# Optimization experiments

Hardware: AMD Instinct MI355X
Metric: run time of the kernel (lower is better)

The kernel has to match this reference:

```python
import jax, jax.numpy as jnp
import numpy as np


def _antideriv_tanh(t):
    # int tanh dx = |x| + log1p(exp(-2|x|))  (numerically stable)
    a = jnp.abs(t)
    return a + jnp.log1p(jnp.exp(-2.0 * a))


def _deriv_tanh(t):
    th = jnp.tanh(t)
    return 1.0 - th * th


def setup_inputs() -> dict:
    key = jax.random.key(0)
    ks = jax.random.split(key, 9)
    d, m, nTh, r, nex = 63, 256, 3, 10, 4096
    x = jax.random.normal(ks[0], (nex, d + 1), dtype=jnp.float32)
    W0 = jax.random.normal(ks[1], (m, d + 1), dtype=jnp.float32) / jnp.sqrt(float(d + 1))
    b0 = jax.random.normal(ks[2], (m,), dtype=jnp.float32) * 0.1
    Wd = jax.random.normal(ks[3], (nTh - 1, m, m), dtype=jnp.float32) / jnp.sqrt(float(m))
    bd = jax.random.normal(ks[4], (nTh - 1, m), dtype=jnp.float32) * 0.1
    wv = jax.random.normal(ks[5], (m,), dtype=jnp.float32)
    A = jax.random.normal(ks[6], (r, d + 1), dtype=jnp.float32) / jnp.sqrt(float(d + 1))
    cw = jax.random.normal(ks[7], (d + 1,), dtype=jnp.float32) * 0.1
    cb = jax.random.normal(ks[8], (), dtype=jnp.float32) * 0.1
    return {"x": x, "W0": W0, "b0": b0, "Wd": Wd, "bd": bd, "wv": wv, "A": A, "cw": cw, "cb": cb}


def reference(x, W0, b0, Wd, bd, wv, A, cw, cb):
    """Phi.trHess: returns (grad of Phi wrt x, trace of Hessian of Phi), shapes [nex, d+1], [nex]."""
    nTh = Wd.shape[0] + 1
    h = 1.0 / (nTh - 1)
    m = W0.shape[0]
    nex = x.shape[0]
    d = x.shape[1] - 1

    symA = A.T @ A                                  # [d+1, d+1]

    # ---- forward propagation of ResNN, keeping hidden states u and preactivations ----
    opening = x @ W0.T + b0                         # [nex, m]
    u = [_antideriv_tanh(opening)]
    pre = []                                        # preactivations of layers 1..nTh-1
    feat = u[0]
    for i in range(1, nTh):
        p = feat @ Wd[i - 1].T + bd[i - 1]          # [nex, m]
        pre.append(p)
        feat = feat + h * _antideriv_tanh(p)
        u.append(feat)

    tanhopen = jnp.tanh(opening)                    # [nex, m]

    # ---- backward z chain (Eq. 11): gradient of w'N(x) wrt x ----
    z = [None] * nTh
    for i in range(nTh - 1, 0, -1):
        term = wv[:, None] if i == nTh - 1 else z[i + 1]      # [m,1] or [m,nex]
        z[i] = term + h * (Wd[i - 1].T @ (jnp.tanh(pre[i - 1]).T * term))
    z0 = W0.T @ (tanhopen.T * z[1])                 # [d+1, nex]
    grad = z0 + symA @ x.T + cw[:, None]            # [d+1, nex]

    # ---- trace of Hessian (Eq. 13) ----
    Kopen = W0[:, :d]                               # [m, d]  (spatial part of opening weight)
    temp = _deriv_tanh(opening.T) * z[1]            # [m, nex]
    # sum_{m,d} temp[m,n] * Kopen[m,d]^2
    trH = jnp.einsum('mn,m->n', temp, jnp.sum(Kopen * Kopen, axis=1))

    Jac = Kopen[:, :, None] * tanhopen.T[:, None, :]          # [m, d, nex]
    for i in range(1, nTh):
        KJ = (Wd[i - 1] @ Jac.reshape(m, d * nex)).reshape(m, d, nex)
        term = wv[:, None] if i == nTh - 1 else z[i + 1]
        p = pre[i - 1].T                             # [m, nex]
        t_i = jnp.einsum('mn,mdn->n', _deriv_tanh(p) * term, KJ * KJ)
        trH = trH + h * t_i
        Jac = Jac + h * jnp.tanh(p)[:, None, :] * KJ

    trH = trH + jnp.trace(symA[:d, :d])
    return grad.T, trH
```

## Files before the change

kernel.cpp:

```cpp
#include <hip/hip_runtime.h>
#include <hip/hip_bf16.h>

#define NEX 4096
#define M   256
#define NM  (NEX*M)

typedef __attribute__((ext_vector_type(8))) short short8;
typedef __attribute__((ext_vector_type(16))) float floatx16;
typedef __attribute__((ext_vector_type(4))) unsigned short ushort4v;

__device__ inline unsigned short f2bfu(float x) {
    __hip_bfloat16 h = __float2bfloat16(x);
    union { __hip_bfloat16 b; unsigned short u; } cv; cv.b = h;
    return cv.u;
}
__device__ inline float bfu2f(unsigned short u) {
    union { unsigned short u; __hip_bfloat16 b; } cv; cv.u = u;
    return __bfloat162float(cv.b);
}

__global__ void k_prep(const float* __restrict__ Wd, const float* __restrict__ W0,
                       const float* __restrict__ A,
                       unsigned short* __restrict__ FB,
                       unsigned short* __restrict__ FBT,
                       unsigned short* __restrict__ FW0,
                       unsigned short* __restrict__ FWT,
                       unsigned short* __restrict__ FSA,
                       float* __restrict__ FA,
                       float* __restrict__ ksq, float* __restrict__ trace) {
    int b = blockIdx.x, t = threadIdx.x;
    int lane = t & 63, l31 = lane & 31, lhi = lane >> 5;
    if (b < 64) {
        int combo = b*4 + (t >> 6);
        int l = combo >> 7, rest = combo & 127;
        int mtile = rest >> 4, kstep = rest & 15;
        const float* src = Wd + l*65536 + (mtile*32 + l31)*256 + kstep*16 + lhi*8;
        int off = l*65536 + (mtile*16 + kstep)*512 + lane*8;
        #pragma unroll
        for (int e = 0; e < 8; ++e) FB[off+e] = f2bfu(src[e]);
    } else if (b < 128) {
        int combo = (b-64)*4 + (t >> 6);
        int l = combo >> 7, rest = combo & 127;
        int kt = rest >> 4, ms = rest & 15;
        const float* src = Wd + l*65536 + (ms*16 + lhi*8)*256 + kt*32 + l31;
        int off = l*65536 + (kt*16 + ms)*512 + lane*8;
        #pragma unroll
        for (int e = 0; e < 8; ++e) FBT[off+e] = f2bfu(src[e*256]);
    } else if (b < 136) {
        int combo = (b-128)*4 + (t >> 6);
        int mt = combo >> 2, ks = combo & 3;
        const float* src = W0 + (mt*32 + l31)*64 + ks*16 + lhi*8;
        int off = combo*512 + lane*8;
        #pragma unroll
        for (int e = 0; e < 8; ++e) FW0[off+e] = f2bfu(src[e]);
    } else if (b < 144) {
        int combo = (b-136)*4 + (t >> 6);
        int ct = combo >> 4, ms = combo & 15;
        const float* src = W0 + (ms*16 + lhi*8)*64 + ct*32 + l31;
        int off = combo*512 + lane*8;
        #pragma unroll
        for (int e = 0; e < 8; ++e) FWT[off+e] = f2bfu(src[e*64]);
    } else if (b < 146) {
        int combo = (b-144)*4 + (t >> 6);
        int ct = combo >> 2, ks = combo & 3;
        int c = ct*32 + l31;
        int off = combo*512 + lane*8;
        #pragma unroll
        for (int e = 0; e < 8; ++e) {
            int j = ks*16 + lhi*8 + e;
            float s = 0.f;
            #pragma unroll
            for (int r = 0; r < 10; ++r) s += A[r*64+c] * A[r*64+j];
            FSA[off+e] = f2bfu(s);
        }
    } else if (b == 146) {
        float s = 0.f;
        for (int dd = 0; dd < 63; dd++) { float v = W0[t*64+dd]; s += v*v; }
        ksq[t] = s;
        float p = 0.f;
        for (int idx = t; idx < 630; idx += 256) {
            int r = idx / 63, i = idx % 63;
            float v = A[r*64+i]; p += v*v;
        }
        for (int off = 32; off; off >>= 1) p += __shfl_down(p, off, 64);
        __shared__ float red[4];
        if ((t & 63) == 0) red[t >> 6] = p;
        __syncthreads();
        if (t == 0) trace[0] = red[0]+red[1]+red[2]+red[3];
    } else {
        int q = (b-147)*256 + t;
        int tl = q & 63, frag = q >> 6;
        int d  = (frag >> 4)*32 + (tl & 31);
        int m0 = (frag & 15)*16 + (tl >> 5)*8;
        float* dst = FA + q*8;
        #pragma unroll
        for (int e = 0; e < 8; ++e)
            dst[e] = (d == 63) ? 0.f : W0[(m0 + e)*64 + d];
    }
}

__global__ __launch_bounds__(512, 2) void k_fb(
        const float* __restrict__ x, const float* __restrict__ b0,
        const float* __restrict__ bd, const float* __restrict__ wv,
        const float* __restrict__ cw,
        const unsigned short* __restrict__ FW0,
        const unsigned short* __restrict__ FB,
        const unsigned short* __restrict__ FBT,
        const unsigned short* __restrict__ FWT,
        const unsigned short* __restrict__ FSA,
        float* __restrict__ tanhopen, float* __restrict__ tp0g,
        float* __restrict__ tp1g, float* __restrict__ z2T, float* __restrict__ z1T,
        float* __restrict__ out) {
    __shared__ __align__(16) unsigned short Buh[8192], Bul[8192];
    __shared__ __align__(16) unsigned short Bxh[2048], Bxl[2048];
    __shared__ __align__(16) float bounce[8224];
    __shared__ float b0s[256], bd0s[256], bd1s[256], wvs[256], cws[64];
    int n0 = blockIdx.x * 32, t = threadIdx.x;
    int lane = t & 63, w = t >> 6, l31 = lane & 31, lhi = lane >> 5;

    if (t < 256) { b0s[t]=b0[t]; bd0s[t]=bd[t]; bd1s[t]=bd[256+t]; wvs[t]=wv[t]; }
    if (t < 64) cws[t] = cw[t];
    if (t < 256) {
        int tl = t & 63;
        int ex = tl & 31, k0 = (t >> 6)*16 + (tl >> 5)*8;
        const float* xp = x + (n0+ex)*64 + k0;
        short8 h8, l8;
        #pragma unroll
        for (int e = 0; e < 8; ++e) {
            float v = xp[e];
            unsigned short h = f2bfu(v);
            h8[e] = (short)h; l8[e] = (short)f2bfu(v - bfu2f(h));
        }
        *reinterpret_cast<short8*>(&Bxh[t*8]) = h8;
        *reinterpret_cast<short8*>(&Bxl[t*8]) = l8;
    }
    __syncthreads();

#define MROW(r) (w*32 + ((r)&3) + 8*((r)>>2) + 4*lhi)

#define MFMA2(AH, BH, BL) do { \
    acc = __builtin_amdgcn_mfma_f32_32x32x16_bf16(AH, BH, acc, 0, 0, 0); \
    acc = __builtin_amdgcn_mfma_f32_32x32x16_bf16(AH, BL, acc, 0, 0, 0); \
} while (0)

#define GEMM256(PH) do { \
    for (int ks = 0; ks < 16; ++ks) { \
        short8 Ah = *reinterpret_cast<const short8*>(PH + (w*16+ks)*512 + lane*8); \
        short8 Bh = *reinterpret_cast<const short8*>(&Buh[(ks*64+lane)*8]); \
        short8 Bl = *reinterpret_cast<const short8*>(&Bul[(ks*64+lane)*8]); \
        MFMA2(Ah, Bh, Bl); \
    } \
} while (0)

#define EPILOGUE(SVAL, DST, BVAL) do { \
    __syncthreads(); \
    _Pragma("unroll") \
    for (int r = 0; r < 16; ++r) bounce[l31*257 + MROW(r)] = SVAL[r]; \
    _Pragma("unroll") \
    for (int g = 0; g < 4; ++g) { \
        int ks_ = w*2 + (g>>1); \
        int lp_ = (g&1)*32 + l31; \
        int base_ = (ks_*64 + lp_)*8 + 4*lhi; \
        ushort4v h4, l4; \
        _Pragma("unroll") \
        for (int q = 0; q < 4; ++q) { \
            float v_ = BVAL[g*4+q]; \
            unsigned short h_ = f2bfu(v_); \
            h4[q] = h_; l4[q] = f2bfu(v_ - bfu2f(h_)); \
        } \
        *reinterpret_cast<ushort4v*>(&Buh[base_]) = h4; \
        *reinterpret_cast<ushort4v*>(&Bul[base_]) = l4; \
    } \
    __syncthreads(); \
    _Pragma("unroll") \
    for (int i = 0; i < 16; ++i) { \
        int f = t + i*512; int ex_ = f >> 8, m_ = f & 255; \
        DST[(n0+ex_)*256 + m_] = bounce[ex_*257 + m_]; \
    } \
} while (0)

    floatx16 acc;
    float sv[16], u0v[16], tp0v[16], z2v[16], cf[16];

    #pragma unroll
    for (int r = 0; r < 16; ++r) acc[r] = 0.f;
    #pragma unroll
    for (int ks = 0; ks < 4; ++ks) {
        short8 Ah = *reinterpret_cast<const short8*>(FW0 + (w*4+ks)*512 + lane*8);
        short8 Bh = *reinterpret_cast<const short8*>(&Bxh[(ks*64+lane)*8]);
        short8 Bl = *reinterpret_cast<const short8*>(&Bxl[(ks*64+lane)*8]);
        MFMA2(Ah, Bh, Bl);
    }
    #pragma unroll
    for (int r = 0; r < 16; ++r) {
        float p = acc[r] + b0s[MROW(r)];
        float a = fabsf(p);
        float e = __expf(-2.f*a);
        float th = (1.f - e) * __builtin_amdgcn_rcpf(1.f + e);
        sv[r] = __builtin_copysignf(th, p);
        u0v[r] = a + __logf(1.f + e);
    }
    EPILOGUE(sv, tanhopen, u0v);

    #pragma unroll
    for (int r = 0; r < 16; ++r) acc[r] = 0.f;
    GEMM256(FB);
    #pragma unroll
    for (int r = 0; r < 16; ++r) {
        float p = acc[r] + bd0s[MROW(r)];
        float a = fabsf(p);
        float e = __expf(-2.f*a);
        float th = (1.f - e) * __builtin_amdgcn_rcpf(1.f + e);
        tp0v[r] = __builtin_copysignf(th, p);
        u0v[r] += 0.5f*(a + __logf(1.f + e));
    }
    EPILOGUE(tp0v, tp0g, u0v);

    #pragma unroll
    for (int r = 0; r < 16; ++r) acc[r] = 0.f;
    GEMM256(FB + 65536);
    #pragma unroll
    for (int r = 0; r < 16; ++r) {
        float p = acc[r] + bd1s[MROW(r)];
        float a = fabsf(p);
        float e = __expf(-2.f*a);
        float th = (1.f - e) * __builtin_amdgcn_rcpf(1.f + e);
        cf[r] = __builtin_copysignf(th, p);
        z2v[r] = cf[r] * wvs[MROW(r)];
    }
    EPILOGUE(cf, tp1g, z2v);

    #pragma unroll
    for (int r = 0; r < 16; ++r) acc[r] = 0.f;
    GEMM256(FBT + 65536);
    #pragma unroll
    for (int r = 0; r < 16; ++r) {
        z2v[r] = wvs[MROW(r)] + 0.5f*acc[r];
        cf[r] = tp0v[r] * z2v[r];
    }
    EPILOGUE(z2v, z2T, cf);

    #pragma unroll
    for (int r = 0; r < 16; ++r) acc[r] = 0.f;
    GEMM256(FBT);
    #pragma unroll
    for (int r = 0; r < 16; ++r) {
        z2v[r] += 0.5f*acc[r];
        cf[r] = sv[r] * z2v[r];
    }
    EPILOGUE(z2v, z1T, cf);

    {
        int ct = w >> 2, seg = w & 3;
        #pragma unroll
        for (int r = 0; r < 16; ++r) acc[r] = 0.f;
        #pragma unroll
        for (int k2 = 0; k2 < 4; ++k2) {
            int ms = seg*4 + k2;
            short8 Ah = *reinterpret_cast<const short8*>(FWT + (ct*16+ms)*512 + lane*8);
            short8 Bh = *reinterpret_cast<const short8*>(&Buh[(ms*64+lane)*8]);
            short8 Bl = *reinterpret_cast<const short8*>(&Bul[(ms*64+lane)*8]);
            MFMA2(Ah, Bh, Bl);
        }
        if (seg == 0) {
            #pragma unroll
            for (int ks = 0; ks < 4; ++ks) {
                short8 Ah = *reinterpret_cast<const short8*>(FSA + (ct*4+ks)*512 + lane*8);
                short8 Bh = *reinterpret_cast<const short8*>(&Bxh[(ks*64+lane)*8]);
                short8 Bl = *reinterpret_cast<const short8*>(&Bxl[(ks*64+lane)*8]);
                MFMA2(Ah, Bh, Bl);
            }
        }
        __syncthreads();
        float* gpart = bounce;
        #pragma unroll
        for (int r = 0; r < 16; ++r) gpart[w*1024 + (2*r+lhi)*32 + l31] = acc[r];
        __syncthreads();
        int o0 = t*4, ex = o0 >> 6, c0 = o0 & 63;
        float4 gv;
        #pragma unroll
        for (int jj = 0; jj < 4; ++jj) {
            int c = c0 + jj;
            int ctx = c >> 5, cr = c & 31;
            int lh = (cr >> 2) & 1;
            int rr = (cr & 3) | ((cr >> 3) << 2);
            float s = cws[c];
            #pragma unroll
            for (int sg = 0; sg < 4; ++sg)
                s += gpart[(ctx*4+sg)*1024 + (2*rr+lh)*32 + ex];
            gv[jj] = s;
        }
        *reinterpret_cast<float4*>(&out[(n0+ex)*64 + c0]) = gv;
    }
#undef MROW
#undef MFMA2
#undef GEMM256
#undef EPILOGUE
}

__global__ __launch_bounds__(256, 3) void k_heavy_mfma(
        const float* __restrict__ tanhopen, const float* __restrict__ tp0,
        const float* __restrict__ tp1, const float* __restrict__ z2T,
        const float* __restrict__ z1T, const float* __restrict__ wv,
        const float* __restrict__ FA, const unsigned short* __restrict__ FB,
        const float* __restrict__ ksq, const float* __restrict__ trace,
        float* __restrict__ outTrH) {
    __shared__ __align__(16) unsigned short Bf[16384];
    __shared__ float ss[256], tp0s[256], w1s[256], w2s[256];
    __shared__ float red[4];
    int n = blockIdx.x, t = threadIdx.x;
    int lane = t & 63, w = t >> 6, l31 = lane & 31, lhi = lane >> 5;

    float sv = tanhopen[n*256 + t];
    float a0 = tp0[n*256 + t];
    float a1 = tp1[n*256 + t];
    ss[t] = sv;
    tp0s[t] = a0;
    w1s[t] = (1.f - a0*a0) * z2T[n*256 + t];
    w2s[t] = (1.f - a1*a1) * wv[t];
    float tot = (1.f - sv*sv) * z1T[n*256 + t] * ksq[t];
    __syncthreads();

    #pragma unroll
    for (int i = 0; i < 8; ++i) {
        int q = t + i*256;
        int frag = q >> 6, tl = q & 63;
        int k0 = (frag & 15)*16 + (tl >> 5)*8;
        const float* fp = FA + q*8;
        short8 v8;
        #pragma unroll
        for (int e = 0; e < 8; ++e)
            v8[e] = (short)f2bfu(fp[e] * ss[k0 + e]);
        *reinterpret_cast<short8*>(&Bf[q*8]) = v8;
    }
    __syncthreads();

    floatx16 acc[2][2];
    int mt0 = w*2, mt1 = w*2 + 1;
    float wtot = 0.f;

    #pragma unroll
    for (int jm = 0; jm < 2; ++jm)
        #pragma unroll
        for (int dh = 0; dh < 2; ++dh)
            #pragma unroll
            for (int r = 0; r < 16; ++r) acc[jm][dh][r] = 0.f;

    for (int ks = 0; ks < 16; ++ks) {
        short8 A0 = *reinterpret_cast<const short8*>(FB + (mt0*16 + ks)*512 + lane*8);
        short8 A1 = *reinterpret_cast<const short8*>(FB + (mt1*16 + ks)*512 + lane*8);
        short8 B0 = *reinterpret_cast<const short8*>(&Bf[((ks)*64 + lane)*8]);
        short8 B1 = *reinterpret_cast<const short8*>(&Bf[((16 + ks)*64 + lane)*8]);
        acc[0][0] = __builtin_amdgcn_mfma_f32_32x32x16_bf16(A0, B0, acc[0][0], 0, 0, 0);
        acc[0][1] = __builtin_amdgcn_mfma_f32_32x32x16_bf16(A0, B1, acc[0][1], 0, 0, 0);
        acc[1][0] = __builtin_amdgcn_mfma_f32_32x32x16_bf16(A1, B0, acc[1][0], 0, 0, 0);
        acc[1][1] = __builtin_amdgcn_mfma_f32_32x32x16_bf16(A1, B1, acc[1][1], 0, 0, 0);
    }
    __syncthreads();

    #pragma unroll
    for (int jm = 0; jm < 2; ++jm) {
        int mt = w*2 + jm;
        #pragma unroll
        for (int g = 0; g < 4; ++g) {
            float w1m[4], tm[4];
            #pragma unroll
            for (int q = 0; q < 4; ++q) {
                int m = mt*32 + 8*g + q + 4*lhi;
                w1m[q] = 0.5f * w1s[m];
                tm[q]  = 0.5f * tp0s[m];
            }
            #pragma unroll
            for (int dh = 0; dh < 2; ++dh) {
                int base = ((dh*16 + mt*2 + (g >> 1))*64
                            + ((g & 1)*32 + l31))*8 + 4*lhi;
                ushort4v old = *reinterpret_cast<ushort4v*>(&Bf[base]);
                ushort4v nw;
                #pragma unroll
                for (int q = 0; q < 4; ++q) {
                    float v = acc[jm][dh][4*g + q];
                    wtot += w1m[q] * v * v;
                    nw[q] = f2bfu(bfu2f(old[q]) + tm[q] * v);
                }
                *reinterpret_cast<ushort4v*>(&Bf[base]) = nw;
            }
        }
    }
    __syncthreads();

    #pragma unroll
    for (int jm = 0; jm < 2; ++jm)
        #pragma unroll
        for (int dh = 0; dh < 2; ++dh)
            #pragma unroll
            for (int r = 0; r < 16; ++r) acc[jm][dh][r] = 0.f;

    const unsigned short* FB1 = FB + 65536;
    for (int ks = 0; ks < 16; ++ks) {
        short8 A0 = *reinterpret_cast<const short8*>(FB1 + (mt0*16 + ks)*512 + lane*8);
        short8 A1 = *reinterpret_cast<const short8*>(FB1 + (mt1*16 + ks)*512 + lane*8);
        short8 B0 = *reinterpret_cast<const short8*>(&Bf[((ks)*64 + lane)*8]);
        short8 B1 = *reinterpret_cast<const short8*>(&Bf[((16 + ks)*64 + lane)*8]);
        acc[0][0] = __builtin_amdgcn_mfma_f32_32x32x16_bf16(A0, B0, acc[0][0], 0, 0, 0);
        acc[0][1] = __builtin_amdgcn_mfma_f32_32x32x16_bf16(A0, B1, acc[0][1], 0, 0, 0);
        acc[1][0] = __builtin_amdgcn_mfma_f32_32x32x16_bf16(A1, B0, acc[1][0], 0, 0, 0);
        acc[1][1] = __builtin_amdgcn_mfma_f32_32x32x16_bf16(A1, B1, acc[1][1], 0, 0, 0);
    }

    #pragma unroll
    for (int jm = 0; jm < 2; ++jm)
        #pragma unroll
        for (int g = 0; g < 4; ++g)
            #pragma unroll
            for (int q = 0; q < 4; ++q) {
                int m = (w*2 + jm)*32 + 8*g + q + 4*lhi;
                float w2m = 0.5f * w2s[m];
                float v0 = acc[jm][0][4*g + q], v1 = acc[jm][1][4*g + q];
                wtot += w2m * (v0*v0 + v1*v1);
            }

    tot += wtot;

    for (int off = 32; off; off >>= 1) tot += __shfl_down(tot, off, 64);
    if (lane == 0) red[w] = tot;
    __syncthreads();
    if (t == 0) outTrH[n] = red[0] + red[1] + red[2] + red[3] + trace[0];
}


extern "C" void kernel_launch(void* const* d_in, const int* in_sizes, int n_in,
                              void* d_out, int out_size, void* d_ws, size_t ws_size,
                              hipStream_t stream) {
    const float* x   = (const float*)d_in[0];
    const float* W0  = (const float*)d_in[1];
    const float* b0  = (const float*)d_in[2];
    const float* Wd  = (const float*)d_in[3];
    const float* bd  = (const float*)d_in[4];
    const float* wv  = (const float*)d_in[5];
    const float* A   = (const float*)d_in[6];
    const float* cw  = (const float*)d_in[7];
    float* out = (float*)d_out;
    float* ws  = (float*)d_ws;

    float* tanhopen = ws;
    float* tp0  = tanhopen + NM;
    float* tp1  = tp0 + NM;
    float* z2T  = tp1 + NM;
    float* z1T  = z2T + NM;
    float* FA   = z1T + NM;
    float* ksq  = FA + 16384;
    float* trace= ksq + 256;
    unsigned short* FB  = (unsigned short*)(trace + 4);
    unsigned short* FBT = FB + 131072;
    unsigned short* FW0 = FBT + 131072;
    unsigned short* FWT = FW0 + 16384;
    unsigned short* FSA = FWT + 16384;

    k_prep<<<155, 256, 0, stream>>>(Wd, W0, A, FB, FBT, FW0, FWT, FSA,
                                    FA, ksq, trace);
    k_fb<<<NEX/32, 512, 0, stream>>>(x, b0, bd, wv, cw,
                                     FW0, FB, FBT, FWT, FSA,
                                     tanhopen, tp0, tp1, z2T, z1T, out);
    k_heavy_mfma<<<NEX, 256, 0, stream>>>(tanhopen, tp0, tp1, z2T, z1T, wv,
                                          FA, FB, ksq, trace, out + NEX*64);
}
```

Measured before the change: 121.1 us.

## Split heavy trace kernel across 8 waves with software-pipelined MFMA loads

Doubles the block size of the per-sample trace kernel from 4 to 8 waves, each wave now owning one 32-row M tile instead of two, which halves accumulator registers per wave. The MFMA loops are unrolled with double-buffered A/B fragment loads, and the first A fragments of the second GEMM are prefetched before the barrier. The aim is more waves in flight and better latency hiding of global and LDS loads. The cost is more threads per block sharing the same LDS and barriers, and half the threads sit idle during the initial staging.

```diff
diff --git a/kernel.cpp b/kernel.cpp
--- a/kernel.cpp
+++ b/kernel.cpp
@@ -298,7 +298,7 @@
 #undef EPILOGUE
 }
 
-__global__ __launch_bounds__(256, 3) void k_heavy_mfma(
+__global__ __launch_bounds__(512, 4) void k_heavy_mfma(
         const float* __restrict__ tanhopen, const float* __restrict__ tp0,
         const float* __restrict__ tp1, const float* __restrict__ z2T,
         const float* __restrict__ z1T, const float* __restrict__ wv,
@@ -307,25 +307,28 @@
         float* __restrict__ outTrH) {
     __shared__ __align__(16) unsigned short Bf[16384];
     __shared__ float ss[256], tp0s[256], w1s[256], w2s[256];
-    __shared__ float red[4];
+    __shared__ float red[8];
     int n = blockIdx.x, t = threadIdx.x;
     int lane = t & 63, w = t >> 6, l31 = lane & 31, lhi = lane >> 5;
 
-    float sv = tanhopen[n*256 + t];
-    float a0 = tp0[n*256 + t];
-    float a1 = tp1[n*256 + t];
-    ss[t] = sv;
-    tp0s[t] = a0;
-    w1s[t] = (1.f - a0*a0) * z2T[n*256 + t];
-    w2s[t] = (1.f - a1*a1) * wv[t];
-    float tot = (1.f - sv*sv) * z1T[n*256 + t] * ksq[t];
+    float tot = 0.f;
+    if (t < 256) {
+        float sv = tanhopen[n*256 + t];
+        float a0 = tp0[n*256 + t];
+        float a1 = tp1[n*256 + t];
+        ss[t] = sv;
+        tp0s[t] = a0;
+        w1s[t] = (1.f - a0*a0) * z2T[n*256 + t];
+        w2s[t] = (1.f - a1*a1) * wv[t];
+        tot = (1.f - sv*sv) * z1T[n*256 + t] * ksq[t];
+    }
     __syncthreads();
 
     #pragma unroll
-    for (int i = 0; i < 8; ++i) {
-        int q = t + i*256;
-        int frag = q >> 6, tl = q & 63;
-        int k0 = (frag & 15)*16 + (tl >> 5)*8;
+    for (int i = 0; i < 4; ++i) {
+        int q = t + i*512;
+        int frag = q >> 6;
+        int k0 = (frag & 15)*16 + ((q & 63) >> 5)*8;
         const float* fp = FA + q*8;
         short8 v8;
         #pragma unroll
@@ -335,96 +338,127 @@
     }
     __syncthreads();
 
-    floatx16 acc[2][2];
-    int mt0 = w*2, mt1 = w*2 + 1;
+    floatx16 acc[2];
+    int mt = w;
     float wtot = 0.f;
 
-    #pragma unroll
-    for (int jm = 0; jm < 2; ++jm)
-        #pragma unroll
-        for (int dh = 0; dh < 2; ++dh)
-            #pragma unroll
-            for (int r = 0; r < 16; ++r) acc[jm][dh][r] = 0.f;
-
-    for (int ks = 0; ks < 16; ++ks) {
-        short8 A0 = *reinterpret_cast<const short8*>(FB + (mt0*16 + ks)*512 + lane*8);
-        short8 A1 = *reinterpret_cast<const short8*>(FB + (mt1*16 + ks)*512 + lane*8);
-        short8 B0 = *reinterpret_cast<const short8*>(&Bf[((ks)*64 + lane)*8]);
-        short8 B1 = *reinterpret_cast<const short8*>(&Bf[((16 + ks)*64 + lane)*8]);
-        acc[0][0] = __builtin_amdgcn_mfma_f32_32x32x16_bf16(A0, B0, acc[0][0], 0, 0, 0);
-        acc[0][1] = __builtin_amdgcn_mfma_f32_32x32x16_bf16(A0, B1, acc[0][1], 0, 0, 0);
-        acc[1][0] = __builtin_amdgcn_mfma_f32_32x32x16_bf16(A1, B0, acc[1][0], 0, 0, 0);
-        acc[1][1] = __builtin_amdgcn_mfma_f32_32x32x16_bf16(A1, B1, acc[1][1], 0, 0, 0);
-    }
+    const unsigned short* pA = FB + mt*16*512 + lane*8;
+    const unsigned short* qB0 = &Bf[lane*8];
+    const unsigned short* qB1 = &Bf[(16*64 + lane)*8];
+
+#define LD8(P, KS) (*reinterpret_cast<const short8*>((P) + (KS)*512))
+#define MFMA2H(A_, B0_, B1_) do { \
+    acc[0] = __builtin_amdgcn_mfma_f32_32x32x16_bf16(A_, B0_, acc[0], 0, 0, 0); \
+    acc[1] = __builtin_amdgcn_mfma_f32_32x32x16_bf16(A_, B1_, acc[1], 0, 0, 0); \
+} while (0)
+
+    #pragma unroll
+    for (int dh = 0; dh < 2; ++dh)
+        #pragma unroll
+        for (int r = 0; r < 16; ++r) acc[dh][r] = 0.f;
+
+    {
+        short8 Aa = LD8(pA, 0);
+        short8 B0a = LD8(qB0, 0), B1a = LD8(qB1, 0);
+        short8 Ab, B0b, B1b;
+        #pragma unroll
+        for (int k2 = 0; k2 < 8; ++k2) {
+            int ksn = 2*k2 + 1;
+            Ab = LD8(pA, ksn);
+            B0b = LD8(qB0, ksn);
+            B1b = LD8(qB1, ksn);
+            MFMA2H(Aa, B0a, B1a);
+            if (k2 < 7) {
+                int ksm = 2*k2 + 2;
+                Aa = LD8(pA, ksm);
+                B0a = LD8(qB0, ksm);
+                B1a = LD8(qB1, ksm);
+            }
+            MFMA2H(Ab, B0b, B1b);
+        }
+    }
+
+    const unsigned short* pC = FB + 65536 + mt*16*512 + lane*8;
+    short8 nA0 = LD8(pC, 0);
+    short8 nA1 = LD8(pC, 1);
+
     __syncthreads();
 
     #pragma unroll
-    for (int jm = 0; jm < 2; ++jm) {
-        int mt = w*2 + jm;
-        #pragma unroll
-        for (int g = 0; g < 4; ++g) {
-            float w1m[4], tm[4];
+    for (int g = 0; g < 4; ++g) {
+        float w1m[4], tm[4];
+        #pragma unroll
+        for (int q = 0; q < 4; ++q) {
+            int m = mt*32 + 8*g + q + 4*lhi;
+            w1m[q] = 0.5f * w1s[m];
+            tm[q]  = 0.5f * tp0s[m];
+        }
+        #pragma unroll
+        for (int dh = 0; dh < 2; ++dh) {
+            int base = ((dh*16 + mt*2 + (g >> 1))*64
+                        + ((g & 1)*32 + l31))*8 + 4*lhi;
+            ushort4v old = *reinterpret_cast<ushort4v*>(&Bf[base]);
+            ushort4v nw;
             #pragma unroll
             for (int q = 0; q < 4; ++q) {
-                int m = mt*32 + 8*g + q + 4*lhi;
-                w1m[q] = 0.5f * w1s[m];
-                tm[q]  = 0.5f * tp0s[m];
+                float v = acc[dh][4*g + q];
+                wtot += w1m[q] * v * v;
+                nw[q] = f2bfu(bfu2f(old[q]) + tm[q] * v);
             }
-            #pragma unroll
-            for (int dh = 0; dh < 2; ++dh) {
-                int base = ((dh*16 + mt*2 + (g >> 1))*64
-                            + ((g & 1)*32 + l31))*8 + 4*lhi;
-                ushort4v old = *reinterpret_cast<ushort4v*>(&Bf[base]);
-                ushort4v nw;
-                #pragma unroll
-                for (int q = 0; q < 4; ++q) {
-                    float v = acc[jm][dh][4*g + q];
-                    wtot += w1m[q] * v * v;
-                    nw[q] = f2bfu(bfu2f(old[q]) + tm[q] * v);
-                }
-                *reinterpret_cast<ushort4v*>(&Bf[base]) = nw;
+            *reinterpret_cast<ushort4v*>(&Bf[base]) = nw;
+        }
+    }
+    __syncthreads();
+
+    #pragma unroll
+    for (int dh = 0; dh < 2; ++dh)
+        #pragma unroll
+        for (int r = 0; r < 16; ++r) acc[dh][r] = 0.f;
+
+    {
+        short8 Aa = nA0;
+        short8 B0a = LD8(qB0, 0), B1a = LD8(qB1, 0);
+        short8 Ab = nA1, B0b, B1b;
+        #pragma unroll
+        for (int k2 = 0; k2 < 8; ++k2) {
+            int ksn = 2*k2 + 1;
+            if (k2 > 0) Ab = LD8(pC, ksn);
+            B0b = LD8(qB0, ksn);
+            B1b = LD8(qB1, ksn);
+            MFMA2H(Aa, B0a, B1a);
+            if (k2 < 7) {
+                int ksm = 2*k2 + 2;
+                Aa = LD8(pC, ksm);
+                B0a = LD8(qB0, ksm);
+                B1a = LD8(qB1, ksm);
             }
-        }
-    }
-    __syncthreads();
-
-    #pragma unroll
-    for (int jm = 0; jm < 2; ++jm)
-        #pragma unroll
-        for (int dh = 0; dh < 2; ++dh)
-            #pragma unroll
-            for (int r = 0; r < 16; ++r) acc[jm][dh][r] = 0.f;
-
-    const unsigned short* FB1 = FB + 65536;
-    for (int ks = 0; ks < 16; ++ks) {
-        short8 A0 = *reinterpret_cast<const short8*>(FB1 + (mt0*16 + ks)*512 + lane*8);
-        short8 A1 = *reinterpret_cast<const short8*>(FB1 + (mt1*16 + ks)*512 + lane*8);
-        short8 B0 = *reinterpret_cast<const short8*>(&Bf[((ks)*64 + lane)*8]);
-        short8 B1 = *reinterpret_cast<const short8*>(&Bf[((16 + ks)*64 + lane)*8]);
-        acc[0][0] = __builtin_amdgcn_mfma_f32_32x32x16_bf16(A0, B0, acc[0][0], 0, 0, 0);
-        acc[0][1] = __builtin_amdgcn_mfma_f32_32x32x16_bf16(A0, B1, acc[0][1], 0, 0, 0);
-        acc[1][0] = __builtin_amdgcn_mfma_f32_32x32x16_bf16(A1, B0, acc[1][0], 0, 0, 0);
-        acc[1][1] = __builtin_amdgcn_mfma_f32_32x32x16_bf16(A1, B1, acc[1][1], 0, 0, 0);
-    }
-
-    #pragma unroll
-    for (int jm = 0; jm < 2; ++jm)
-        #pragma unroll
-        for (int g = 0; g < 4; ++g)
-            #pragma unroll
-            for (int q = 0; q < 4; ++q) {
-                int m = (w*2 + jm)*32 + 8*g + q + 4*lhi;
-                float w2m = 0.5f * w2s[m];
-                float v0 = acc[jm][0][4*g + q], v1 = acc[jm][1][4*g + q];
-                wtot += w2m * (v0*v0 + v1*v1);
-            }
+            MFMA2H(Ab, B0b, B1b);
+        }
+    }
+#undef MFMA2H
+#undef LD8
+
+    #pragma unroll
+    for (int g = 0; g < 4; ++g)
+        #pragma unroll
+        for (int q = 0; q < 4; ++q) {
+            int m = mt*32 + 8*g + q + 4*lhi;
+            float w2m = 0.5f * w2s[m];
+            float v0 = acc[0][4*g + q], v1 = acc[1][4*g + q];
+            wtot += w2m * (v0*v0 + v1*v1);
+        }
 
     tot += wtot;
 
     for (int off = 32; off; off >>= 1) tot += __shfl_down(tot, off, 64);
     if (lane == 0) red[w] = tot;
     __syncthreads();
-    if (t == 0) outTrH[n] = red[0] + red[1] + red[2] + red[3] + trace[0];
+    if (t == 0) {
+        float s = trace[0];
+        #pragma unroll
+        for (int i = 0; i < 8; ++i) s += red[i];
+        outTrH[n] = s;
+    }
 }
 
 
@@ -461,6 +495,6 @@
     k_fb<<<NEX/32, 512, 0, stream>>>(x, b0, bd, wv, cw,
                                      FW0, FB, FBT, FWT, FSA,
                                      tanhopen, tp0, tp1, z2T, z1T, out);
-    k_heavy_mfma<<<NEX, 256, 0, stream>>>(tanhopen, tp0, tp1, z2T, z1T, wv,
+    k_heavy_mfma<<<NEX, 512, 0, stream>>>(tanhopen, tp0, tp1, z2T, z1T, wv,
                                           FA, FB, ksq, trace, out + NEX*64);
 }
```

After: 120.5 us. No clear change (-0.5%).
